# Kernel optimization log

Measured on AMD Instinct MI355X. Metric: run time of the kernel, lower is better.

Reference implementation:

```python
import jax, jax.numpy as jnp
import numpy as np

TEMPERATURE = 0.5
DIFFUSION_STEPS = 10
N = 8192
C = 128
E = 262144  # includes N self-loops to guarantee degree >= 1


def setup_inputs() -> dict:
    key = jax.random.key(0)
    k1, k2, k3, k4 = jax.random.split(key, 4)
    embeddings = jax.random.normal(k1, (N, C), dtype=jnp.float32)
    # self-loops first, then random edges
    src = jnp.concatenate([jnp.arange(N), jax.random.randint(k2, (E - N,), 0, N)])
    dst = jnp.concatenate([jnp.arange(N), jax.random.randint(k3, (E - N,), 0, N)])
    edge_index = jnp.stack([src, dst]).astype(jnp.int64)
    rand_indices = jax.random.permutation(k4, N).astype(jnp.int64)
    return {"embeddings": embeddings, "edge_index": edge_index, "rand_indices": rand_indices}


def reference(embeddings, edge_index, rand_indices):
    n = embeddings.shape[0]
    # dense adjacency via scatter-set (matches torch index assignment: duplicates -> 1)
    adj = jnp.zeros((n, n), dtype=embeddings.dtype).at[edge_index[0], edge_index[1]].set(1.0)
    d_inv_sqrt = jnp.power(adj.sum(axis=1), -0.5)  # [n]
    # D^-1/2 A D^-1/2 without materializing diag matmuls
    diffusion = d_inv_sqrt[:, None] * adj * d_inv_sqrt[None, :]
    for _ in range(DIFFUSION_STEPS):
        embeddings = diffusion @ embeddings
    pos_pairs = jnp.einsum('nc,nc->n', embeddings[edge_index[0]], embeddings[edge_index[1]]) / TEMPERATURE
    pos_loss = -jnp.mean(jax.nn.log_sigmoid(pos_pairs))
    neg_pairs = jnp.einsum('nc,nc->n', embeddings, embeddings[rand_indices]) / TEMPERATURE
    neg_loss = -jnp.mean(jax.nn.log_sigmoid(-neg_pairs))
    return pos_loss + neg_loss
```

## Files before the change

kernel.cpp:

```cpp
#include <hip/hip_runtime.h>
#include <math.h>

#define N        8192
#define C        128
#define E_TOTAL  262144
#define WPR      256
#define INV_TEMP 2.0f
#define STEPS    10
#define S_ELL    96
#define S_PAD    104
#define POS_BLOCKS 2048
#define NEG_BLOCKS 128

#define OFF_D       1024
#define OFF_CNT     (OFF_D + 32768)
#define OFF_PPOS    (OFF_CNT + 32768)
#define OFF_PNEG    (OFF_PPOS + POS_BLOCKS * 4)
#define OFF_ELL     (OFF_PNEG + 1024)
#define OFF_BITMAP  (OFF_ELL + N * S_PAD * 8)
#define BITMAP_BYTES (N * WPR * 4)
#define OFF_BUFA    OFF_BITMAP
#define OFF_BUFB    (OFF_BUFA + N * C * 2)

typedef unsigned int   uint;
typedef unsigned short ushort;

__device__ __forceinline__ float bflo(uint u) { return __uint_as_float(u << 16); }
__device__ __forceinline__ float bfhi(uint u) { return __uint_as_float(u & 0xffff0000u); }
__device__ __forceinline__ ushort f2bf(float f) {
    uint u = __float_as_uint(f);
    return (ushort)((u + 0x7fffu + ((u >> 16) & 1u)) >> 16);
}
__device__ __forceinline__ float dot_u(uint a, uint b) {
    return bflo(a) * bflo(b) + bfhi(a) * bfhi(b);
}
__device__ __forceinline__ float log_sigmoid(float z) {
    return fminf(z, 0.0f) - log1pf(expf(-fabsf(z)));
}

__global__ void scatter_edges_kernel(const int* __restrict__ ei,
                                     unsigned int* __restrict__ bm) {
    int e = blockIdx.x * blockDim.x + threadIdx.x;
    if (e >= E_TOTAL) return;
    int s = ei[e];
    int t = ei[E_TOTAL + e];
    atomicOr(&bm[s * WPR + (t >> 5)], 1u << (t & 31));
}

__global__ void degree_kernel(const unsigned int* __restrict__ bm,
                              float* __restrict__ dinv) {
    int row = blockIdx.x;
    int lane = threadIdx.x;
    const unsigned int* p = bm + row * WPR;
    int cnt = 0;
    for (int w = lane; w < WPR; w += 64) cnt += __popc(p[w]);
    for (int off = 32; off > 0; off >>= 1) cnt += __shfl_down(cnt, off, 64);
    if (lane == 0) dinv[row] = 1.0f / sqrtf((float)cnt);
}

__global__ void build_ell_kernel(const unsigned int* __restrict__ bm,
                                 const float* __restrict__ dinv,
                                 int* __restrict__ cnt,
                                 int2* __restrict__ ell) {
    int row = blockIdx.x;
    int lane = threadIdx.x;
    const unsigned int* p = bm + row * WPR;
    unsigned int w[4];
    int c = 0;
    for (int i = 0; i < 4; ++i) { w[i] = p[lane * 4 + i]; c += __popc(w[i]); }
    int inc = c;
    for (int off = 1; off < 64; off <<= 1) {
        int v = __shfl_up(inc, off, 64);
        if (lane >= off) inc += v;
    }
    int pos = inc - c;
    int total = __shfl(inc, 63, 64);
    float dr = dinv[row];
    int2* er = ell + row * S_PAD;
    for (int i = 0; i < 4; ++i) {
        unsigned int word = w[i];
        int jbase = (lane * 4 + i) << 5;
        while (word) {
            int b = __ffs(word) - 1;
            word &= word - 1;
            int j = jbase + b;
            if (pos < S_ELL) {
                int2 pr; pr.x = j; pr.y = __float_as_int(dr * dinv[j]);
                er[pos] = pr;
            }
            ++pos;
        }
    }
    int ncap = (total < S_ELL) ? total : S_ELL;
    int npad = (ncap + 7) & ~7;
    if (lane < npad - ncap) {
        int2 pr; pr.x = row; pr.y = 0;
        er[ncap + lane] = pr;
    }
    if (lane == 0) cnt[row] = npad;
}

__global__ __launch_bounds__(256) void spmm_step_kernel(
        const int* __restrict__ cnt,
        const int2* __restrict__ ell,
        const void* __restrict__ xin,
        ushort* __restrict__ y,
        int first) {
    int wid  = threadIdx.x >> 6;
    int lane = threadIdx.x & 63;
    int row  = blockIdx.x * 4 + wid;
    int npad = cnt[row];
    int qw   = lane >> 4;
    int l16  = lane & 15;
    const int2* er = ell + row * S_PAD;
    float a0 = 0.f, a1 = 0.f, a2 = 0.f, a3 = 0.f;
    float a4 = 0.f, a5 = 0.f, a6 = 0.f, a7 = 0.f;
    if (first) {
        const float* x = (const float*)xin;
        for (int k = 0; k < npad; k += 8) {
            int2 p0 = er[k + qw];
            int2 p1 = er[k + 4 + qw];
            float w0 = __int_as_float(p0.y);
            float w1 = __int_as_float(p1.y);
            const float* r0 = x + p0.x * C + l16 * 8;
            const float* r1 = x + p1.x * C + l16 * 8;
            float4 u0a = *(const float4*)r0, u0b = *(const float4*)(r0 + 4);
            float4 u1a = *(const float4*)r1, u1b = *(const float4*)(r1 + 4);
            a0 += w0 * u0a.x; a1 += w0 * u0a.y; a2 += w0 * u0a.z; a3 += w0 * u0a.w;
            a4 += w0 * u0b.x; a5 += w0 * u0b.y; a6 += w0 * u0b.z; a7 += w0 * u0b.w;
            a0 += w1 * u1a.x; a1 += w1 * u1a.y; a2 += w1 * u1a.z; a3 += w1 * u1a.w;
            a4 += w1 * u1b.x; a5 += w1 * u1b.y; a6 += w1 * u1b.z; a7 += w1 * u1b.w;
        }
    } else {
        const ushort* x = (const ushort*)xin;
        for (int k = 0; k < npad; k += 8) {
            int2 p0 = er[k + qw];
            int2 p1 = er[k + 4 + qw];
            float w0 = __int_as_float(p0.y);
            float w1 = __int_as_float(p1.y);
            uint4 u0 = *(const uint4*)(x + p0.x * C + l16 * 8);
            uint4 u1 = *(const uint4*)(x + p1.x * C + l16 * 8);
            a0 += w0 * bflo(u0.x); a1 += w0 * bfhi(u0.x);
            a2 += w0 * bflo(u0.y); a3 += w0 * bfhi(u0.y);
            a4 += w0 * bflo(u0.z); a5 += w0 * bfhi(u0.z);
            a6 += w0 * bflo(u0.w); a7 += w0 * bfhi(u0.w);
            a0 += w1 * bflo(u1.x); a1 += w1 * bfhi(u1.x);
            a2 += w1 * bflo(u1.y); a3 += w1 * bfhi(u1.y);
            a4 += w1 * bflo(u1.z); a5 += w1 * bfhi(u1.z);
            a6 += w1 * bflo(u1.w); a7 += w1 * bfhi(u1.w);
        }
    }
    a0 += __shfl_xor(a0, 16, 64); a0 += __shfl_xor(a0, 32, 64);
    a1 += __shfl_xor(a1, 16, 64); a1 += __shfl_xor(a1, 32, 64);
    a2 += __shfl_xor(a2, 16, 64); a2 += __shfl_xor(a2, 32, 64);
    a3 += __shfl_xor(a3, 16, 64); a3 += __shfl_xor(a3, 32, 64);
    a4 += __shfl_xor(a4, 16, 64); a4 += __shfl_xor(a4, 32, 64);
    a5 += __shfl_xor(a5, 16, 64); a5 += __shfl_xor(a5, 32, 64);
    a6 += __shfl_xor(a6, 16, 64); a6 += __shfl_xor(a6, 32, 64);
    a7 += __shfl_xor(a7, 16, 64); a7 += __shfl_xor(a7, 32, 64);
    if (qw == 0) {
        uint4 o;
        o.x = (uint)f2bf(a0) | ((uint)f2bf(a1) << 16);
        o.y = (uint)f2bf(a2) | ((uint)f2bf(a3) << 16);
        o.z = (uint)f2bf(a4) | ((uint)f2bf(a5) << 16);
        o.w = (uint)f2bf(a6) | ((uint)f2bf(a7) << 16);
        *(uint4*)(y + row * C + l16 * 8) = o;
    }
}

__global__ void loss_kernel(const ushort* __restrict__ x,
                            const int* __restrict__ ei,
                            const int* __restrict__ ridx,
                            float* __restrict__ ppos,
                            float* __restrict__ pneg) {
    __shared__ float wsum[4];
    int lane = threadIdx.x & 63;
    int g    = lane >> 2;
    int q    = lane & 3;
    float sum = 0.0f;
    if (blockIdx.x < POS_BLOCKS) {
        int wave = (blockIdx.x * blockDim.x + threadIdx.x) >> 6;
        int nwaves = (POS_BLOCKS * 256) >> 6;
        for (int base = wave * 16; base < E_TOTAL; base += nwaves * 16) {
            int e = base + g;
            int s = ei[e];
            int t = ei[E_TOTAL + e];
            const uint4* ps = (const uint4*)(x + s * C + q * 32);
            const uint4* pt = (const uint4*)(x + t * C + q * 32);
            uint4 s0 = ps[0], s1 = ps[1], s2 = ps[2], s3 = ps[3];
            uint4 t0 = pt[0], t1 = pt[1], t2 = pt[2], t3 = pt[3];
            float p = dot_u(s0.x, t0.x) + dot_u(s0.y, t0.y) + dot_u(s0.z, t0.z) + dot_u(s0.w, t0.w)
                    + dot_u(s1.x, t1.x) + dot_u(s1.y, t1.y) + dot_u(s1.z, t1.z) + dot_u(s1.w, t1.w)
                    + dot_u(s2.x, t2.x) + dot_u(s2.y, t2.y) + dot_u(s2.z, t2.z) + dot_u(s2.w, t2.w)
                    + dot_u(s3.x, t3.x) + dot_u(s3.y, t3.y) + dot_u(s3.z, t3.z) + dot_u(s3.w, t3.w);
            p += __shfl_xor(p, 1, 64);
            p += __shfl_xor(p, 2, 64);
            if (q == 0) sum += log_sigmoid(p * INV_TEMP);
        }
    } else {
        int bi = blockIdx.x - POS_BLOCKS;
        int wave = (bi * blockDim.x + threadIdx.x) >> 6;
        int nwaves = (NEG_BLOCKS * 256) >> 6;
        for (int base = wave * 16; base < N; base += nwaves * 16) {
            int i = base + g;
            int t = ridx[i];
            const uint4* ps = (const uint4*)(x + i * C + q * 32);
            const uint4* pt = (const uint4*)(x + t * C + q * 32);
            uint4 s0 = ps[0], s1 = ps[1], s2 = ps[2], s3 = ps[3];
            uint4 t0 = pt[0], t1 = pt[1], t2 = pt[2], t3 = pt[3];
            float p = dot_u(s0.x, t0.x) + dot_u(s0.y, t0.y) + dot_u(s0.z, t0.z) + dot_u(s0.w, t0.w)
                    + dot_u(s1.x, t1.x) + dot_u(s1.y, t1.y) + dot_u(s1.z, t1.z) + dot_u(s1.w, t1.w)
                    + dot_u(s2.x, t2.x) + dot_u(s2.y, t2.y) + dot_u(s2.z, t2.z) + dot_u(s2.w, t2.w)
                    + dot_u(s3.x, t3.x) + dot_u(s3.y, t3.y) + dot_u(s3.z, t3.z) + dot_u(s3.w, t3.w);
            p += __shfl_xor(p, 1, 64);
            p += __shfl_xor(p, 2, 64);
            if (q == 0) sum += log_sigmoid(-p * INV_TEMP);
        }
    }
    sum += __shfl_xor(sum, 4, 64);
    sum += __shfl_xor(sum, 8, 64);
    sum += __shfl_xor(sum, 16, 64);
    sum += __shfl_xor(sum, 32, 64);
    if (lane == 0) wsum[threadIdx.x >> 6] = sum;
    __syncthreads();
    if (threadIdx.x == 0) {
        float v = (wsum[0] + wsum[1]) + (wsum[2] + wsum[3]);
        if (blockIdx.x < POS_BLOCKS) ppos[blockIdx.x] = v;
        else                         pneg[blockIdx.x - POS_BLOCKS] = v;
    }
}

__global__ void finalize_kernel(const float* __restrict__ ppos,
                                const float* __restrict__ pneg,
                                float* __restrict__ out) {
    __shared__ float red[256];
    int t = threadIdx.x;
    float s = 0.0f;
    for (int i = t; i < POS_BLOCKS; i += 256) s += ppos[i];
    float sn = (t < NEG_BLOCKS) ? pneg[t] : 0.0f;
    red[t] = s * (-1.0f / (float)E_TOTAL) + sn * (-1.0f / (float)N);
    __syncthreads();
    for (int off = 128; off > 0; off >>= 1) {
        if (t < off) red[t] += red[t + off];
        __syncthreads();
    }
    if (t == 0) out[0] = red[0];
}

extern "C" void kernel_launch(void* const* d_in, const int* in_sizes, int n_in,
                              void* d_out, int out_size, void* d_ws, size_t ws_size,
                              hipStream_t stream) {
    (void)in_sizes; (void)n_in; (void)out_size; (void)ws_size;

    const float* emb_in = (const float*)d_in[0];
    const int*   ei     = (const int*)d_in[1];
    const int*   ridx   = (const int*)d_in[2];
    float* out = (float*)d_out;

    char* ws = (char*)d_ws;
    float*        dinv = (float*)(ws + OFF_D);
    int*          cnt  = (int*)(ws + OFF_CNT);
    float*        ppos = (float*)(ws + OFF_PPOS);
    float*        pneg = (float*)(ws + OFF_PNEG);
    int2*         ell  = (int2*)(ws + OFF_ELL);
    unsigned int* bm   = (unsigned int*)(ws + OFF_BITMAP);
    ushort*       bufA = (ushort*)(ws + OFF_BUFA);
    ushort*       bufB = (ushort*)(ws + OFF_BUFB);
    ushort*       buf[2] = {bufA, bufB};

    hipMemsetAsync(bm, 0, BITMAP_BYTES, stream);

    scatter_edges_kernel<<<E_TOTAL / 256, 256, 0, stream>>>(ei, bm);
    degree_kernel<<<N, 64, 0, stream>>>(bm, dinv);
    build_ell_kernel<<<N, 64, 0, stream>>>(bm, dinv, cnt, ell);

    for (int s = 0; s < STEPS; ++s) {
        const void* xs = (s == 0) ? (const void*)emb_in : (const void*)buf[s & 1];
        ushort* yd = buf[(s + 1) & 1];
        spmm_step_kernel<<<N / 4, 256, 0, stream>>>(cnt, ell, xs, yd, s == 0 ? 1 : 0);
    }
    const ushort* emb = buf[STEPS & 1];

    loss_kernel<<<POS_BLOCKS + NEG_BLOCKS, 256, 0, stream>>>(emb, ei, ridx, ppos, pneg);
    finalize_kernel<<<1, 256, 0, stream>>>(ppos, pneg, out);
}
```

Before: 191.0 us.

## Factor symmetric normalization out of SpMM, store column-only ELL in shared memory

The symmetric normalization is rewritten as an iteration on a D^-1/2-scaled state. Each intermediate step scales its output row by d^-1 (the last step by d^-1/2), so the ELL only needs column indices, not (col, weight) pairs. The inner loop becomes pure adds. The separate degree kernel is merged into the ELL build, and each block stages its four rows' column lists in LDS. Padding now points at a zeroed extra row. This halves index traffic and removes one launch, but it relies on the bf16 rescaled intermediates staying accurate.

```diff
diff --git a/kernel.cpp b/kernel.cpp
--- a/kernel.cpp
+++ b/kernel.cpp
@@ -8,19 +8,19 @@
 #define INV_TEMP 2.0f
 #define STEPS    10
 #define S_ELL    96
-#define S_PAD    104
+#define ZROW     N
 #define POS_BLOCKS 2048
 #define NEG_BLOCKS 128
 
-#define OFF_D       1024
-#define OFF_CNT     (OFF_D + 32768)
+#define OFF_DINV    1024
+#define OFF_CNT     (OFF_DINV + 32768)
 #define OFF_PPOS    (OFF_CNT + 32768)
 #define OFF_PNEG    (OFF_PPOS + POS_BLOCKS * 4)
 #define OFF_ELL     (OFF_PNEG + 1024)
-#define OFF_BITMAP  (OFF_ELL + N * S_PAD * 8)
+#define OFF_BITMAP  (OFF_ELL + N * S_ELL * 4)
 #define BITMAP_BYTES (N * WPR * 4)
-#define OFF_BUFA    OFF_BITMAP
-#define OFF_BUFB    (OFF_BUFA + N * C * 2)
+#define OFF_BUFA    (OFF_BITMAP + BITMAP_BYTES)
+#define OFF_BUFB    (OFF_BUFA + (N + 1) * C * 2)
 
 typedef unsigned int   uint;
 typedef unsigned short ushort;
@@ -47,21 +47,10 @@
     atomicOr(&bm[s * WPR + (t >> 5)], 1u << (t & 31));
 }
 
-__global__ void degree_kernel(const unsigned int* __restrict__ bm,
-                              float* __restrict__ dinv) {
-    int row = blockIdx.x;
-    int lane = threadIdx.x;
-    const unsigned int* p = bm + row * WPR;
-    int cnt = 0;
-    for (int w = lane; w < WPR; w += 64) cnt += __popc(p[w]);
-    for (int off = 32; off > 0; off >>= 1) cnt += __shfl_down(cnt, off, 64);
-    if (lane == 0) dinv[row] = 1.0f / sqrtf((float)cnt);
-}
-
 __global__ void build_ell_kernel(const unsigned int* __restrict__ bm,
-                                 const float* __restrict__ dinv,
                                  int* __restrict__ cnt,
-                                 int2* __restrict__ ell) {
+                                 int* __restrict__ ellc,
+                                 float* __restrict__ dinvs) {
     int row = blockIdx.x;
     int lane = threadIdx.x;
     const unsigned int* p = bm + row * WPR;
@@ -75,79 +64,82 @@
     }
     int pos = inc - c;
     int total = __shfl(inc, 63, 64);
-    float dr = dinv[row];
-    int2* er = ell + row * S_PAD;
     for (int i = 0; i < 4; ++i) {
         unsigned int word = w[i];
         int jbase = (lane * 4 + i) << 5;
         while (word) {
             int b = __ffs(word) - 1;
             word &= word - 1;
-            int j = jbase + b;
-            if (pos < S_ELL) {
-                int2 pr; pr.x = j; pr.y = __float_as_int(dr * dinv[j]);
-                er[pos] = pr;
-            }
+            if (pos < S_ELL) ellc[row * S_ELL + pos] = jbase + b;
             ++pos;
         }
     }
     int ncap = (total < S_ELL) ? total : S_ELL;
     int npad = (ncap + 7) & ~7;
-    if (lane < npad - ncap) {
-        int2 pr; pr.x = row; pr.y = 0;
-        er[ncap + lane] = pr;
-    }
-    if (lane == 0) cnt[row] = npad;
+    if (lane < npad - ncap)
+        ellc[row * S_ELL + ncap + lane] = ZROW;
+    if (lane == 0) {
+        cnt[row] = ncap;
+        dinvs[row] = rsqrtf((float)total);
+    }
 }
 
 __global__ __launch_bounds__(256) void spmm_step_kernel(
-        const int* __restrict__ cnt,
-        const int2* __restrict__ ell,
-        const void* __restrict__ xin,
-        ushort* __restrict__ y,
-        int first) {
-    int wid  = threadIdx.x >> 6;
-    int lane = threadIdx.x & 63;
-    int row  = blockIdx.x * 4 + wid;
-    int npad = cnt[row];
-    int qw   = lane >> 4;
-    int l16  = lane & 15;
-    const int2* er = ell + row * S_PAD;
-    float a0 = 0.f, a1 = 0.f, a2 = 0.f, a3 = 0.f;
-    float a4 = 0.f, a5 = 0.f, a6 = 0.f, a7 = 0.f;
+        const int* __restrict__ cnt, const int* __restrict__ ellc,
+        const float* __restrict__ dinvs, const void* __restrict__ xin,
+        ushort* __restrict__ y, int first, int last) {
+    __shared__ int   scol[4 * S_ELL];
+    __shared__ int   sn[4];
+    __shared__ float ssc[4];
+    const int tid  = threadIdx.x;
+    const int wid  = tid >> 6;
+    const int lane = tid & 63;
+    const int qw   = lane >> 4;
+    const int l16  = lane & 15;
+
+    for (int i = tid; i < 4 * S_ELL; i += 256)
+        scol[i] = ellc[blockIdx.x * 4 * S_ELL + i];
+    if (tid < 4) {
+        int row = blockIdx.x * 4 + tid;
+        sn[tid] = cnt[row];
+        float ds = dinvs[row];
+        ssc[tid] = last ? ds : ds * ds;
+    }
+    __syncthreads();
+
+    int row = blockIdx.x * 4 + wid;
+    int n = sn[wid];
+    const int* cr = scol + wid * S_ELL;
+    float a0=0.f,a1=0.f,a2=0.f,a3=0.f,a4=0.f,a5=0.f,a6=0.f,a7=0.f;
     if (first) {
         const float* x = (const float*)xin;
-        for (int k = 0; k < npad; k += 8) {
-            int2 p0 = er[k + qw];
-            int2 p1 = er[k + 4 + qw];
-            float w0 = __int_as_float(p0.y);
-            float w1 = __int_as_float(p1.y);
-            const float* r0 = x + p0.x * C + l16 * 8;
-            const float* r1 = x + p1.x * C + l16 * 8;
-            float4 u0a = *(const float4*)r0, u0b = *(const float4*)(r0 + 4);
-            float4 u1a = *(const float4*)r1, u1b = *(const float4*)(r1 + 4);
-            a0 += w0 * u0a.x; a1 += w0 * u0a.y; a2 += w0 * u0a.z; a3 += w0 * u0a.w;
-            a4 += w0 * u0b.x; a5 += w0 * u0b.y; a6 += w0 * u0b.z; a7 += w0 * u0b.w;
-            a0 += w1 * u1a.x; a1 += w1 * u1a.y; a2 += w1 * u1a.z; a3 += w1 * u1a.w;
-            a4 += w1 * u1b.x; a5 += w1 * u1b.y; a6 += w1 * u1b.z; a7 += w1 * u1b.w;
+        for (int k = 0; k < n; k += 8) {
+            int i0 = k + qw, i1 = k + 4 + qw;
+            int   c0 = (i0 < n) ? cr[i0] : row;
+            int   c1 = (i1 < n) ? cr[i1] : row;
+            float w0 = (i0 < n) ? dinvs[c0] : 0.0f;
+            float w1 = (i1 < n) ? dinvs[c1] : 0.0f;
+            const float* r0 = x + c0 * C + l16 * 8;
+            const float* r1 = x + c1 * C + l16 * 8;
+            float4 ua = *(const float4*)r0, ub = *(const float4*)(r0 + 4);
+            float4 va = *(const float4*)r1, vb = *(const float4*)(r1 + 4);
+            a0 += w0 * ua.x + w1 * va.x;  a1 += w0 * ua.y + w1 * va.y;
+            a2 += w0 * ua.z + w1 * va.z;  a3 += w0 * ua.w + w1 * va.w;
+            a4 += w0 * ub.x + w1 * vb.x;  a5 += w0 * ub.y + w1 * vb.y;
+            a6 += w0 * ub.z + w1 * vb.z;  a7 += w0 * ub.w + w1 * vb.w;
         }
     } else {
         const ushort* x = (const ushort*)xin;
+        int npad = (n + 7) & ~7;
         for (int k = 0; k < npad; k += 8) {
-            int2 p0 = er[k + qw];
-            int2 p1 = er[k + 4 + qw];
-            float w0 = __int_as_float(p0.y);
-            float w1 = __int_as_float(p1.y);
-            uint4 u0 = *(const uint4*)(x + p0.x * C + l16 * 8);
-            uint4 u1 = *(const uint4*)(x + p1.x * C + l16 * 8);
-            a0 += w0 * bflo(u0.x); a1 += w0 * bfhi(u0.x);
-            a2 += w0 * bflo(u0.y); a3 += w0 * bfhi(u0.y);
-            a4 += w0 * bflo(u0.z); a5 += w0 * bfhi(u0.z);
-            a6 += w0 * bflo(u0.w); a7 += w0 * bfhi(u0.w);
-            a0 += w1 * bflo(u1.x); a1 += w1 * bfhi(u1.x);
-            a2 += w1 * bflo(u1.y); a3 += w1 * bfhi(u1.y);
-            a4 += w1 * bflo(u1.z); a5 += w1 * bfhi(u1.z);
-            a6 += w1 * bflo(u1.w); a7 += w1 * bfhi(u1.w);
+            int c0 = cr[k + qw];
+            int c1 = cr[k + 4 + qw];
+            uint4 u0 = *(const uint4*)(x + c0 * C + l16 * 8);
+            uint4 u1 = *(const uint4*)(x + c1 * C + l16 * 8);
+            a0 += bflo(u0.x) + bflo(u1.x);  a1 += bfhi(u0.x) + bfhi(u1.x);
+            a2 += bflo(u0.y) + bflo(u1.y);  a3 += bfhi(u0.y) + bfhi(u1.y);
+            a4 += bflo(u0.z) + bflo(u1.z);  a5 += bfhi(u0.z) + bfhi(u1.z);
+            a6 += bflo(u0.w) + bflo(u1.w);  a7 += bfhi(u0.w) + bfhi(u1.w);
         }
     }
     a0 += __shfl_xor(a0, 16, 64); a0 += __shfl_xor(a0, 32, 64);
@@ -159,11 +151,12 @@
     a6 += __shfl_xor(a6, 16, 64); a6 += __shfl_xor(a6, 32, 64);
     a7 += __shfl_xor(a7, 16, 64); a7 += __shfl_xor(a7, 32, 64);
     if (qw == 0) {
+        float sc = ssc[wid];
         uint4 o;
-        o.x = (uint)f2bf(a0) | ((uint)f2bf(a1) << 16);
-        o.y = (uint)f2bf(a2) | ((uint)f2bf(a3) << 16);
-        o.z = (uint)f2bf(a4) | ((uint)f2bf(a5) << 16);
-        o.w = (uint)f2bf(a6) | ((uint)f2bf(a7) << 16);
+        o.x = (uint)f2bf(a0 * sc) | ((uint)f2bf(a1 * sc) << 16);
+        o.y = (uint)f2bf(a2 * sc) | ((uint)f2bf(a3 * sc) << 16);
+        o.z = (uint)f2bf(a4 * sc) | ((uint)f2bf(a5 * sc) << 16);
+        o.w = (uint)f2bf(a6 * sc) | ((uint)f2bf(a7 * sc) << 16);
         *(uint4*)(y + row * C + l16 * 8) = o;
     }
 }
@@ -258,26 +251,29 @@
     float* out = (float*)d_out;
 
     char* ws = (char*)d_ws;
-    float*        dinv = (float*)(ws + OFF_D);
-    int*          cnt  = (int*)(ws + OFF_CNT);
-    float*        ppos = (float*)(ws + OFF_PPOS);
-    float*        pneg = (float*)(ws + OFF_PNEG);
-    int2*         ell  = (int2*)(ws + OFF_ELL);
-    unsigned int* bm   = (unsigned int*)(ws + OFF_BITMAP);
-    ushort*       bufA = (ushort*)(ws + OFF_BUFA);
-    ushort*       bufB = (ushort*)(ws + OFF_BUFB);
+    float*        dinvs = (float*)(ws + OFF_DINV);
+    int*          cnt   = (int*)(ws + OFF_CNT);
+    float*        ppos  = (float*)(ws + OFF_PPOS);
+    float*        pneg  = (float*)(ws + OFF_PNEG);
+    int*          ellc  = (int*)(ws + OFF_ELL);
+    unsigned int* bm    = (unsigned int*)(ws + OFF_BITMAP);
+    ushort*       bufA  = (ushort*)(ws + OFF_BUFA);
+    ushort*       bufB  = (ushort*)(ws + OFF_BUFB);
     ushort*       buf[2] = {bufA, bufB};
 
     hipMemsetAsync(bm, 0, BITMAP_BYTES, stream);
+    hipMemsetAsync(bufA + (size_t)ZROW * C, 0, C * 2, stream);
+    hipMemsetAsync(bufB + (size_t)ZROW * C, 0, C * 2, stream);
 
     scatter_edges_kernel<<<E_TOTAL / 256, 256, 0, stream>>>(ei, bm);
-    degree_kernel<<<N, 64, 0, stream>>>(bm, dinv);
-    build_ell_kernel<<<N, 64, 0, stream>>>(bm, dinv, cnt, ell);
+    build_ell_kernel<<<N, 64, 0, stream>>>(bm, cnt, ellc, dinvs);
 
     for (int s = 0; s < STEPS; ++s) {
         const void* xs = (s == 0) ? (const void*)emb_in : (const void*)buf[s & 1];
         ushort* yd = buf[(s + 1) & 1];
-        spmm_step_kernel<<<N / 4, 256, 0, stream>>>(cnt, ell, xs, yd, s == 0 ? 1 : 0);
+        spmm_step_kernel<<<N / 4, 256, 0, stream>>>(cnt, ellc, dinvs, xs, yd,
+                                                    s == 0 ? 1 : 0,
+                                                    s == STEPS - 1 ? 1 : 0);
     }
     const ushort* emb = buf[STEPS & 1];
 
```

New measurement: 181.6 us. 1.05x faster.
